# Optimization experiments

Hardware: AMD Instinct MI355X
Metric: run time of the kernel (lower is better)

## Reference

```python
import jax, jax.numpy as jnp
import numpy as np


def setup_inputs() -> dict:
    key = jax.random.key(0)
    k1, k2 = jax.random.split(key)
    B, N, M = 8, 8192, 8192
    pred = jax.random.normal(k1, (B, N, 3), dtype=jnp.float32)
    target = jax.random.normal(k2, (B, M, 3), dtype=jnp.float32)
    return {"pred": pred, "target": target}


def reference(pred, target):
    # pairwise squared distances: (B, N, M)
    pred_sq = jnp.sum(pred ** 2, axis=2, keepdims=True)            # (B, N, 1)
    target_sq = jnp.sum(target ** 2, axis=2, keepdims=True)        # (B, M, 1)
    dist = pred_sq + jnp.swapaxes(target_sq, 1, 2) \
           - 2.0 * jnp.einsum('bnd,bmd->bnm', pred, target)
    dist = jnp.maximum(dist, 0.0)
    cd_p2t = jnp.mean(jnp.min(dist, axis=2))   # pred -> target
    cd_t2p = jnp.mean(jnp.min(dist, axis=1))   # target -> pred (bidirectional=True)
    return cd_p2t + cd_t2p
```

## Files before the change

### kernel.cpp

```cpp
#include <hip/hip_runtime.h>
#include <math.h>

#define THREADS  256
#define NPTS     8192
#define BATCH    8
#define ENTRIES  (2 * BATCH * NPTS)
#define ENC_U4   (2 * BATCH * 8 * 2048)
#define ENC_BYTES ((size_t)ENC_U4 * 16)
#define NPLANES  4
#define MINS_BYTES ((size_t)NPLANES * ENTRIES * 4)
#define WS1_BYTES (ENC_BYTES + MINS_BYTES)
#define WS_BYTES  ((size_t)ENTRIES * 4)

typedef __attribute__((ext_vector_type(8)))  short bf16x8;
typedef __attribute__((ext_vector_type(8)))  float f32x8;
typedef __attribute__((ext_vector_type(16))) float f32x16;

union FragCast { uint4 u; bf16x8 v; };

__device__ __forceinline__ unsigned short f2bf(float f) {
    unsigned u = __float_as_uint(f);
    unsigned r = (u + 0x7FFFu + ((u >> 16) & 1u)) >> 16;
    return (unsigned short)r;
}
__device__ __forceinline__ float bf2f(unsigned short h) {
    return __uint_as_float(((unsigned)h) << 16);
}
#define PK(a, b) (((unsigned)(a)) | (((unsigned)(b)) << 16))
#define BF_ONE 0x3F80u

__device__ __forceinline__ void encode_db_point(float x, float y, float z,
                                                uint4& h0, uint4& h1) {
    const float sq = fmaf(x, x, fmaf(y, y, z * z));
    const unsigned short xh = f2bf(x), yh = f2bf(y), zh = f2bf(z);
    const unsigned short xl = f2bf(x - bf2f(xh));
    const unsigned short yl = f2bf(y - bf2f(yh));
    const unsigned short zl = f2bf(z - bf2f(zh));
    const unsigned short sh = f2bf(sq);
    const unsigned short sl = f2bf(sq - bf2f(sh));
    h0 = make_uint4(PK(xh, yh), PK(zh, xl), PK(yl, zl), PK(xh, yh));
    h1 = make_uint4(PK(zh, xl), PK(yl, zl), PK(sh, sl), PK(BF_ONE, BF_ONE));
}

__device__ __forceinline__ bf16x8 make_query_frag(const float* qp, int half) {
    const float x = qp[0], y = qp[1], z = qp[2];
    const float sq = fmaf(x, x, fmaf(y, y, z * z));
    const float wx = -2.0f * x, wy = -2.0f * y, wz = -2.0f * z;
    const unsigned short wxh = f2bf(wx), wyh = f2bf(wy), wzh = f2bf(wz);
    const unsigned short wxl = f2bf(wx - bf2f(wxh));
    const unsigned short wyl = f2bf(wy - bf2f(wyh));
    const unsigned short wzl = f2bf(wz - bf2f(wzh));
    const unsigned short sh  = f2bf(sq);
    const unsigned short sl  = f2bf(sq - bf2f(sh));
    FragCast fc;
    if (half == 0) fc.u = make_uint4(PK(wxh, wyh), PK(wzh, wxh), PK(wyh, wzh), PK(wxl, wyl));
    else           fc.u = make_uint4(PK(wzl, wxl), PK(wyl, wzl), PK(BF_ONE, BF_ONE), PK(sh, sl));
    return fc.v;
}

__global__ __launch_bounds__(THREADS)
void chamfer_encode_kernel(const float* __restrict__ pred,
                           const float* __restrict__ target,
                           uint4* __restrict__ enc,
                           float* __restrict__ out)
{
    const int t   = blockIdx.x * THREADS + threadIdx.x;
    if (t == 0) out[0] = 0.0f;
    const int arr = t >> 16;
    const int rem = t & 0xFFFF;
    const int b   = rem >> 13;
    const int p   = rem & (NPTS - 1);
    const float* src = (arr ? target : pred) + ((size_t)b * NPTS + p) * 3;
    uint4 h0, h1;
    encode_db_point(src[0], src[1], src[2], h0, h1);
    const int T = p >> 5, c = p & 31;
    uint4* base = enc + (size_t)(arr * BATCH + b) * 16384;
    base[T * 64 + c]      = h0;
    base[T * 64 + c + 32] = h1;
}

__global__ __launch_bounds__(THREADS, 4)
void chamfer_mfma4_kernel(const float* __restrict__ pred,
                          const float* __restrict__ target,
                          const uint4* __restrict__ enc,
                          float* __restrict__ mins)
{
    const int bx  = blockIdx.x;
    const int ds  = bx & 3;
    const int qb  = (bx >> 2) & 15;
    const int b   = (bx >> 6) & 7;
    const int dir = bx >> 9;

    const float* qarr = dir ? target : pred;
    const int arr_db  = dir ^ 1;

    const int tid  = threadIdx.x;
    const int ln   = tid & 63;
    const int w    = tid >> 6;
    const int half = ln >> 5;

    const int qbase = qb * 512 + w * 128;
    const size_t qrow = (size_t)b * NPTS;
    bf16x8 bq0 = make_query_frag(qarr + (qrow + qbase +  0 + (ln & 31)) * 3, half);
    bf16x8 bq1 = make_query_frag(qarr + (qrow + qbase + 32 + (ln & 31)) * 3, half);
    bf16x8 bq2 = make_query_frag(qarr + (qrow + qbase + 64 + (ln & 31)) * 3, half);
    bf16x8 bq3 = make_query_frag(qarr + (qrow + qbase + 96 + (ln & 31)) * 3, half);

    const f32x16 zacc = {};
    f32x8 m0, m1, m2, m3;
    #pragma unroll
    for (int i = 0; i < 8; ++i) { m0[i] = INFINITY; m1[i] = INFINITY; m2[i] = INFINITY; m3[i] = INFINITY; }

    const uint4* gbase = enc + (size_t)(arr_db * BATCH + b) * 16384 + ds * 4096 + ln;

    #pragma unroll 2
    for (int jj = 0; jj < 64; ++jj) {
        FragCast a;
        a.u = gbase[jj * 64];
        const f32x16 c0 = __builtin_amdgcn_mfma_f32_32x32x16_bf16(a.v, bq0, zacc, 0, 0, 0);
        #pragma unroll
        for (int i = 0; i < 8; ++i) m0[i] = fminf(fminf(m0[i], c0[2*i]), c0[2*i+1]);
        const f32x16 c1 = __builtin_amdgcn_mfma_f32_32x32x16_bf16(a.v, bq1, zacc, 0, 0, 0);
        #pragma unroll
        for (int i = 0; i < 8; ++i) m1[i] = fminf(fminf(m1[i], c1[2*i]), c1[2*i+1]);
        const f32x16 c2 = __builtin_amdgcn_mfma_f32_32x32x16_bf16(a.v, bq2, zacc, 0, 0, 0);
        #pragma unroll
        for (int i = 0; i < 8; ++i) m2[i] = fminf(fminf(m2[i], c2[2*i]), c2[2*i+1]);
        const f32x16 c3 = __builtin_amdgcn_mfma_f32_32x32x16_bf16(a.v, bq3, zacc, 0, 0, 0);
        #pragma unroll
        for (int i = 0; i < 8; ++i) m3[i] = fminf(fminf(m3[i], c3[2*i]), c3[2*i+1]);
    }

    const int base = ds * ENTRIES + dir * (BATCH * NPTS) + b * NPTS + qbase;
    #pragma unroll
    for (int nb = 0; nb < 4; ++nb) {
        const f32x8& m = (nb == 0) ? m0 : (nb == 1) ? m1 : (nb == 2) ? m2 : m3;
        float r = fminf(fminf(fminf(m[0], m[1]), fminf(m[2], m[3])),
                        fminf(fminf(m[4], m[5]), fminf(m[6], m[7])));
        r = fminf(r, __shfl_xor(r, 32, 64));
        if (ln < 32) mins[base + nb * 32 + ln] = r;
    }
}

__global__ __launch_bounds__(THREADS)
void chamfer_finish4_kernel(const float* __restrict__ mins,
                            float* __restrict__ out,
                            float inv_count)
{
    const int t = blockIdx.x * THREADS + threadIdx.x;
    const float4* p0 = (const float4*)mins;
    const float4* p1 = (const float4*)(mins + ENTRIES);
    const float4* p2 = (const float4*)(mins + 2 * ENTRIES);
    const float4* p3 = (const float4*)(mins + 3 * ENTRIES);
    const float4 a = p0[t], c = p1[t], d = p2[t], e = p3[t];
    float s = fmaxf(fminf(fminf(a.x, c.x), fminf(d.x, e.x)), 0.0f)
            + fmaxf(fminf(fminf(a.y, c.y), fminf(d.y, e.y)), 0.0f)
            + fmaxf(fminf(fminf(a.z, c.z), fminf(d.z, e.z)), 0.0f)
            + fmaxf(fminf(fminf(a.w, c.w), fminf(d.w, e.w)), 0.0f);
    float v = s;
    #pragma unroll
    for (int off = 32; off > 0; off >>= 1)
        v += __shfl_down(v, off, 64);
    __shared__ float wsum[THREADS / 64];
    if ((threadIdx.x & 63) == 0) wsum[threadIdx.x >> 6] = v;
    __syncthreads();
    if (threadIdx.x == 0)
        atomicAdd(out, (wsum[0] + wsum[1] + wsum[2] + wsum[3]) * inv_count);
}

__global__ __launch_bounds__(THREADS, 4)
void chamfer_mfma_kernel(const float* __restrict__ pred,
                         const float* __restrict__ target,
                         unsigned* __restrict__ wskeys)
{
    __shared__ short lds[32 * 64 * 8];
    const int bx  = blockIdx.x;
    const int ds  = bx & 3;
    const int qb  = (bx >> 2) & 15;
    const int b   = (bx >> 6) & 7;
    const int dir = bx >> 9;
    const float* qarr = dir ? target : pred;
    const float* darr = dir ? pred   : target;
    const int tid  = threadIdx.x;
    const int ln   = tid & 63;
    const int w    = tid >> 6;
    const int half = ln >> 5;

    bf16x8 bq[4];
    const int qbase = qb * 512 + w * 128;
    #pragma unroll
    for (int nb = 0; nb < 4; ++nb)
        bq[nb] = make_query_frag(qarr + ((size_t)b * NPTS + qbase + nb * 32 + (ln & 31)) * 3, half);

    float mn[4] = {INFINITY, INFINITY, INFINITY, INFINITY};
    const int range0 = ds * 2048;
    for (int chunk = 0; chunk < 2; ++chunk) {
        #pragma unroll
        for (int it = 0; it < 4; ++it) {
            const int pl = it * THREADS + tid;
            const int p  = range0 + chunk * 1024 + pl;
            const float* tp = darr + ((size_t)b * NPTS + p) * 3;
            uint4 h0, h1;
            encode_db_point(tp[0], tp[1], tp[2], h0, h1);
            const int j = pl >> 5, c = pl & 31;
            *(uint4*)&lds[(j * 64 + c) * 8]      = h0;
            *(uint4*)&lds[(j * 64 + c + 32) * 8] = h1;
        }
        __syncthreads();
        #pragma unroll 4
        for (int j = 0; j < 32; ++j) {
            const bf16x8 a = *(const bf16x8*)&lds[(j * 64 + ln) * 8];
            f32x16 z = {};
            f32x16 c0 = __builtin_amdgcn_mfma_f32_32x32x16_bf16(a, bq[0], z, 0, 0, 0);
            f32x16 c1 = __builtin_amdgcn_mfma_f32_32x32x16_bf16(a, bq[1], z, 0, 0, 0);
            f32x16 c2 = __builtin_amdgcn_mfma_f32_32x32x16_bf16(a, bq[2], z, 0, 0, 0);
            f32x16 c3 = __builtin_amdgcn_mfma_f32_32x32x16_bf16(a, bq[3], z, 0, 0, 0);
            #pragma unroll
            for (int i = 0; i < 16; i += 2) {
                mn[0] = fminf(mn[0], fminf(c0[i], c0[i + 1]));
                mn[1] = fminf(mn[1], fminf(c1[i], c1[i + 1]));
                mn[2] = fminf(mn[2], fminf(c2[i], c2[i + 1]));
                mn[3] = fminf(mn[3], fminf(c3[i], c3[i + 1]));
            }
        }
        __syncthreads();
    }
    const int obase = dir * (BATCH * NPTS) + b * NPTS;
    #pragma unroll
    for (int nb = 0; nb < 4; ++nb) {
        const float o = __shfl_xor(mn[nb], 32, 64);
        const float m = fminf(mn[nb], o);
        if (ln < 32) {
            const unsigned u   = __float_as_uint(m);
            const unsigned key = (u >> 31) ? ~u : (u | 0x80000000u);
            atomicMin(&wskeys[obase + qbase + nb * 32 + ln], key);
        }
    }
}

__global__ __launch_bounds__(THREADS)
void chamfer_finish_kernel(const unsigned* __restrict__ ws,
                           float* __restrict__ out,
                           float inv_count)
{
    const int t = blockIdx.x * THREADS + threadIdx.x;
    const uint4 kk = ((const uint4*)ws)[t];
    float s = 0.0f;
    { const unsigned u = (kk.x >> 31) ? (kk.x ^ 0x80000000u) : ~kk.x; s += fmaxf(__uint_as_float(u), 0.0f); }
    { const unsigned u = (kk.y >> 31) ? (kk.y ^ 0x80000000u) : ~kk.y; s += fmaxf(__uint_as_float(u), 0.0f); }
    { const unsigned u = (kk.z >> 31) ? (kk.z ^ 0x80000000u) : ~kk.z; s += fmaxf(__uint_as_float(u), 0.0f); }
    { const unsigned u = (kk.w >> 31) ? (kk.w ^ 0x80000000u) : ~kk.w; s += fmaxf(__uint_as_float(u), 0.0f); }
    float v = s;
    #pragma unroll
    for (int off = 32; off > 0; off >>= 1)
        v += __shfl_down(v, off, 64);
    __shared__ float wsum[THREADS / 64];
    if ((threadIdx.x & 63) == 0) wsum[threadIdx.x >> 6] = v;
    __syncthreads();
    if (threadIdx.x == 0)
        atomicAdd(out, (wsum[0] + wsum[1] + wsum[2] + wsum[3]) * inv_count);
}

__global__ __launch_bounds__(THREADS, 2)
void chamfer_fallback_kernel(const float* __restrict__ pred,
                             const float* __restrict__ target,
                             float* __restrict__ out,
                             float inv_count)
{
    __shared__ float4 lds[2048];
    const float* q  = (blockIdx.y == 0) ? pred   : target;
    const float* db = (blockIdx.y == 0) ? target : pred;
    const int b = blockIdx.x / (NPTS / THREADS);
    const int n = (blockIdx.x % (NPTS / THREADS)) * THREADS + threadIdx.x;
    const float* qp = q + ((size_t)b * NPTS + n) * 3;
    const float px = qp[0], py = qp[1], pz = qp[2];
    const float npx = -2.0f * px, npy = -2.0f * py, npz = -2.0f * pz;
    const float P = px * px + py * py + pz * pz;
    const float* dbB = db + (size_t)b * NPTS * 3;
    float m0 = INFINITY;
    for (int c0 = 0; c0 < NPTS; c0 += 2048) {
        for (int k = 0; k < 2048 / THREADS; ++k) {
            const int j = k * THREADS + threadIdx.x;
            const float* tp = dbB + (size_t)(c0 + j) * 3;
            const float tx = tp[0], ty = tp[1], tz = tp[2];
            lds[j] = make_float4(tx, ty, tz, tx * tx + ty * ty + tz * tz);
        }
        __syncthreads();
        for (int j = 0; j < 2048; ++j) {
            const float4 T = lds[j];
            m0 = fminf(m0, fmaf(npx, T.x, fmaf(npy, T.y, fmaf(npz, T.z, T.w))));
        }
        __syncthreads();
    }
    float v = fmaxf(P + m0, 0.0f);
    #pragma unroll
    for (int off = 32; off > 0; off >>= 1)
        v += __shfl_down(v, off, 64);
    __shared__ float wsum[THREADS / 64];
    if ((threadIdx.x & 63) == 0) wsum[threadIdx.x >> 6] = v;
    __syncthreads();
    if (threadIdx.x == 0)
        atomicAdd(out, (wsum[0] + wsum[1] + wsum[2] + wsum[3]) * inv_count);
}

extern "C" void kernel_launch(void* const* d_in, const int* in_sizes, int n_in,
                              void* d_out, int out_size, void* d_ws, size_t ws_size,
                              hipStream_t stream) {
    const float* pred   = (const float*)d_in[0];
    const float* target = (const float*)d_in[1];
    float* out = (float*)d_out;
    const float inv_count = 1.0f / (float)(BATCH * NPTS);

    if (ws_size >= WS1_BYTES) {
        uint4* enc  = (uint4*)d_ws;
        float* mins = (float*)((char*)d_ws + ENC_BYTES);
        chamfer_encode_kernel<<<(2 * BATCH * NPTS) / THREADS, THREADS, 0, stream>>>(
            pred, target, enc, out);
        chamfer_mfma4_kernel<<<1024, THREADS, 0, stream>>>(pred, target, enc, mins);
        chamfer_finish4_kernel<<<ENTRIES / (THREADS * 4), THREADS, 0, stream>>>(
            mins, out, inv_count);
    } else if (ws_size >= WS_BYTES) {
        hipMemsetAsync(out, 0, out_size * sizeof(float), stream);
        unsigned* ws = (unsigned*)d_ws;
        hipMemsetAsync(ws, 0xFF, WS_BYTES, stream);
        chamfer_mfma_kernel<<<1024, THREADS, 0, stream>>>(pred, target, ws);
        chamfer_finish_kernel<<<ENTRIES / (THREADS * 4), THREADS, 0, stream>>>(ws, out, inv_count);
    } else {
        hipMemsetAsync(out, 0, out_size * sizeof(float), stream);
        dim3 grid(BATCH * (NPTS / THREADS), 2);
        chamfer_fallback_kernel<<<grid, THREADS, 0, stream>>>(pred, target, out, inv_count);
    }
}
```

Measured before the change: 94.58 us.

## Fuse database point encoding into MFMA kernel via LDS staging

Removes the separate encode kernel and its global workspace buffer. Each block now encodes its 2048 database points into bf16 fragments directly in shared memory, in two 1024-point chunks, then runs the MFMA min-reduction reading fragments from LDS. This saves one kernel launch and a global round-trip of the encoded data. In exchange every block redoes encoding arithmetic that 16 query blocks share, adds __syncthreads barriers, and adds a hipMemsetAsync to zero the output.

```diff
diff --git a/kernel.cpp b/kernel.cpp
--- a/kernel.cpp
+++ b/kernel.cpp
@@ -5,11 +5,8 @@
 #define NPTS     8192
 #define BATCH    8
 #define ENTRIES  (2 * BATCH * NPTS)
-#define ENC_U4   (2 * BATCH * 8 * 2048)
-#define ENC_BYTES ((size_t)ENC_U4 * 16)
 #define NPLANES  4
 #define MINS_BYTES ((size_t)NPLANES * ENTRIES * 4)
-#define WS1_BYTES (ENC_BYTES + MINS_BYTES)
 #define WS_BYTES  ((size_t)ENTRIES * 4)
 
 typedef __attribute__((ext_vector_type(8)))  short bf16x8;
@@ -58,33 +55,13 @@
     return fc.v;
 }
 
-__global__ __launch_bounds__(THREADS)
-void chamfer_encode_kernel(const float* __restrict__ pred,
-                           const float* __restrict__ target,
-                           uint4* __restrict__ enc,
-                           float* __restrict__ out)
-{
-    const int t   = blockIdx.x * THREADS + threadIdx.x;
-    if (t == 0) out[0] = 0.0f;
-    const int arr = t >> 16;
-    const int rem = t & 0xFFFF;
-    const int b   = rem >> 13;
-    const int p   = rem & (NPTS - 1);
-    const float* src = (arr ? target : pred) + ((size_t)b * NPTS + p) * 3;
-    uint4 h0, h1;
-    encode_db_point(src[0], src[1], src[2], h0, h1);
-    const int T = p >> 5, c = p & 31;
-    uint4* base = enc + (size_t)(arr * BATCH + b) * 16384;
-    base[T * 64 + c]      = h0;
-    base[T * 64 + c + 32] = h1;
-}
-
 __global__ __launch_bounds__(THREADS, 4)
-void chamfer_mfma4_kernel(const float* __restrict__ pred,
+void chamfer_mfma5_kernel(const float* __restrict__ pred,
                           const float* __restrict__ target,
-                          const uint4* __restrict__ enc,
                           float* __restrict__ mins)
 {
+    __shared__ short lds[32 * 64 * 8];
+
     const int bx  = blockIdx.x;
     const int ds  = bx & 3;
     const int qb  = (bx >> 2) & 15;
@@ -92,7 +69,7 @@
     const int dir = bx >> 9;
 
     const float* qarr = dir ? target : pred;
-    const int arr_db  = dir ^ 1;
+    const float* darr = dir ? pred   : target;
 
     const int tid  = threadIdx.x;
     const int ln   = tid & 63;
@@ -101,34 +78,57 @@
 
     const int qbase = qb * 512 + w * 128;
     const size_t qrow = (size_t)b * NPTS;
-    bf16x8 bq0 = make_query_frag(qarr + (qrow + qbase +  0 + (ln & 31)) * 3, half);
-    bf16x8 bq1 = make_query_frag(qarr + (qrow + qbase + 32 + (ln & 31)) * 3, half);
-    bf16x8 bq2 = make_query_frag(qarr + (qrow + qbase + 64 + (ln & 31)) * 3, half);
-    bf16x8 bq3 = make_query_frag(qarr + (qrow + qbase + 96 + (ln & 31)) * 3, half);
+    const bf16x8 bq0 = make_query_frag(qarr + (qrow + qbase +  0 + (ln & 31)) * 3, half);
+    const bf16x8 bq1 = make_query_frag(qarr + (qrow + qbase + 32 + (ln & 31)) * 3, half);
+    const bf16x8 bq2 = make_query_frag(qarr + (qrow + qbase + 64 + (ln & 31)) * 3, half);
+    const bf16x8 bq3 = make_query_frag(qarr + (qrow + qbase + 96 + (ln & 31)) * 3, half);
 
     const f32x16 zacc = {};
     f32x8 m0, m1, m2, m3;
     #pragma unroll
     for (int i = 0; i < 8; ++i) { m0[i] = INFINITY; m1[i] = INFINITY; m2[i] = INFINITY; m3[i] = INFINITY; }
 
-    const uint4* gbase = enc + (size_t)(arr_db * BATCH + b) * 16384 + ds * 4096 + ln;
-
-    #pragma unroll 2
-    for (int jj = 0; jj < 64; ++jj) {
-        FragCast a;
-        a.u = gbase[jj * 64];
-        const f32x16 c0 = __builtin_amdgcn_mfma_f32_32x32x16_bf16(a.v, bq0, zacc, 0, 0, 0);
+    const int range0 = ds * 2048;
+
+    for (int chunk = 0; chunk < 2; ++chunk) {
         #pragma unroll
-        for (int i = 0; i < 8; ++i) m0[i] = fminf(fminf(m0[i], c0[2*i]), c0[2*i+1]);
-        const f32x16 c1 = __builtin_amdgcn_mfma_f32_32x32x16_bf16(a.v, bq1, zacc, 0, 0, 0);
-        #pragma unroll
-        for (int i = 0; i < 8; ++i) m1[i] = fminf(fminf(m1[i], c1[2*i]), c1[2*i+1]);
-        const f32x16 c2 = __builtin_amdgcn_mfma_f32_32x32x16_bf16(a.v, bq2, zacc, 0, 0, 0);
-        #pragma unroll
-        for (int i = 0; i < 8; ++i) m2[i] = fminf(fminf(m2[i], c2[2*i]), c2[2*i+1]);
-        const f32x16 c3 = __builtin_amdgcn_mfma_f32_32x32x16_bf16(a.v, bq3, zacc, 0, 0, 0);
-        #pragma unroll
-        for (int i = 0; i < 8; ++i) m3[i] = fminf(fminf(m3[i], c3[2*i]), c3[2*i+1]);
+        for (int it = 0; it < 4; ++it) {
+            const int pl = it * THREADS + tid;
+            const int p  = range0 + chunk * 1024 + pl;
+            const float* tp = darr + ((size_t)b * NPTS + p) * 3;
+            uint4 h0, h1;
+            encode_db_point(tp[0], tp[1], tp[2], h0, h1);
+            const int j = pl >> 5, c = pl & 31;
+            *(uint4*)&lds[(j * 64 + c) * 8]      = h0;
+            *(uint4*)&lds[(j * 64 + c + 32) * 8] = h1;
+        }
+        __syncthreads();
+
+        #pragma unroll 2
+        for (int j = 0; j < 32; ++j) {
+            const bf16x8 a = *(const bf16x8*)&lds[(j * 64 + ln) * 8];
+            {
+                const f32x16 c = __builtin_amdgcn_mfma_f32_32x32x16_bf16(a, bq0, zacc, 0, 0, 0);
+                #pragma unroll
+                for (int i = 0; i < 8; ++i) m0[i] = fminf(fminf(m0[i], c[2*i]), c[2*i+1]);
+            }
+            {
+                const f32x16 c = __builtin_amdgcn_mfma_f32_32x32x16_bf16(a, bq1, zacc, 0, 0, 0);
+                #pragma unroll
+                for (int i = 0; i < 8; ++i) m1[i] = fminf(fminf(m1[i], c[2*i]), c[2*i+1]);
+            }
+            {
+                const f32x16 c = __builtin_amdgcn_mfma_f32_32x32x16_bf16(a, bq2, zacc, 0, 0, 0);
+                #pragma unroll
+                for (int i = 0; i < 8; ++i) m2[i] = fminf(fminf(m2[i], c[2*i]), c[2*i+1]);
+            }
+            {
+                const f32x16 c = __builtin_amdgcn_mfma_f32_32x32x16_bf16(a, bq3, zacc, 0, 0, 0);
+                #pragma unroll
+                for (int i = 0; i < 8; ++i) m3[i] = fminf(fminf(m3[i], c[2*i]), c[2*i+1]);
+            }
+        }
+        __syncthreads();
     }
 
     const int base = ds * ENTRIES + dir * (BATCH * NPTS) + b * NPTS + qbase;
@@ -311,12 +311,10 @@
     float* out = (float*)d_out;
     const float inv_count = 1.0f / (float)(BATCH * NPTS);
 
-    if (ws_size >= WS1_BYTES) {
-        uint4* enc  = (uint4*)d_ws;
-        float* mins = (float*)((char*)d_ws + ENC_BYTES);
-        chamfer_encode_kernel<<<(2 * BATCH * NPTS) / THREADS, THREADS, 0, stream>>>(
-            pred, target, enc, out);
-        chamfer_mfma4_kernel<<<1024, THREADS, 0, stream>>>(pred, target, enc, mins);
+    if (ws_size >= MINS_BYTES) {
+        float* mins = (float*)d_ws;
+        hipMemsetAsync(out, 0, out_size * sizeof(float), stream);
+        chamfer_mfma5_kernel<<<1024, THREADS, 0, stream>>>(pred, target, mins);
         chamfer_finish4_kernel<<<ENTRIES / (THREADS * 4), THREADS, 0, stream>>>(
             mins, out, inv_count);
     } else if (ws_size >= WS_BYTES) {
```

New measurement: 92.11 us. 2.6% less time.
